# Optimization experiments

Measured on AMD Instinct MI355X. Metric: run time of the kernel, lower is better.

## Reference

```python
import jax, jax.numpy as jnp
import numpy as np

B, S, N, E = 16, 2048, 256, 4096      # batch, tokens, max entities, edges per sample
H, LD, ETR = 512, 16, 768             # hidden_size, label_emb_dim, transformer dim
D = H + LD                            # graph_dim = 528
C1 = 3                                # num_edge_classes + 1
GL = 2                                # gcn_layers
NLBL = 15                             # num_node_classes + 2


def setup_inputs() -> dict:
    key = jax.random.key(0)
    ks = jax.random.split(key, 14)
    s = 0.02
    inp = {}
    inp["emb"] = jax.random.normal(ks[0], (B, S, ETR), jnp.float32)
    inp["ent_indices"] = jax.random.randint(ks[1], (B, S), 0, N + 1)
    inp["ent_labels"] = jax.random.randint(ks[2], (B, N), 0, NLBL)
    inp["edge_index"] = jax.random.randint(ks[3], (B, 2, E), 0, N + 1)
    inp["edge_attr"] = jax.random.randint(ks[4], (B, E), 0, C1)
    inp["cands"] = jax.random.randint(ks[5], (B, N + 1, N + 1), 0, 2).astype(bool)
    inp["W_red"] = jax.random.normal(ks[6], (ETR, H), jnp.float32) * s
    inp["b_red"] = jnp.zeros((H,), jnp.float32)
    inp["emb_label_tbl"] = jax.random.normal(ks[7], (NLBL, LD), jnp.float32) * s
    inp["W_gcn"] = jax.random.normal(ks[8], (C1, GL, D, D), jnp.float32) * s
    inp["b_gcn"] = jnp.zeros((C1, GL, D), jnp.float32)
    inp["W_head"] = jax.random.normal(ks[9], (D, D), jnp.float32) * s
    inp["b_head"] = jnp.zeros((D,), jnp.float32)
    inp["W_tail"] = jax.random.normal(ks[10], (D, D), jnp.float32) * s
    inp["b_tail"] = jnp.zeros((D,), jnp.float32)
    inp["W_out"] = jax.random.normal(ks[11], (D, C1), jnp.float32) * s
    inp["b_out"] = jnp.zeros((C1,), jnp.float32)
    return inp


def _gcn_layer(x, src, dst, w_e, W, b):
    """PyG GCNConv with edge weights w_e (0/1 relation mask) and self loops.
    x: [n, D]; src/dst: [E]; aggregation flow source->target."""
    n = x.shape[0]
    h = x @ W
    deg = jax.ops.segment_sum(w_e, dst, num_segments=n) + 1.0  # +1 self loop
    dinv = jax.lax.rsqrt(deg)
    coef = w_e * dinv[src] * dinv[dst]                         # D^-1/2 A D^-1/2
    agg = jax.ops.segment_sum(coef[:, None] * h[src], dst, num_segments=n)
    return agg + h / deg[:, None] + b                          # self-loop norm = 1/deg


def reference(emb, ent_indices, ent_labels, edge_index, edge_attr, cands,
              W_red, b_red, emb_label_tbl, W_gcn, b_gcn,
              W_head, b_head, W_tail, b_tail, W_out, b_out):
    n_nodes = cands.shape[1]  # max_num_ent + 1
    # fc_reduction of frozen transformer embeddings
    red = emb @ W_red + b_red                                   # [B,S,H]
    # tag-based segment aggregation: max over (mask * emb) == max(segment_max, 0)
    seg_max = jax.vmap(lambda e, ids: jax.ops.segment_max(e, ids, num_segments=n_nodes))(red, ent_indices)
    ent_hidden = jnp.maximum(seg_max, 0.0).at[:, 0, :].set(0.0)  # tag 0 stays zero
    # label embeddings: tag t uses ent_labels[:, t-1]; zeroed where label==0
    lab = emb_label_tbl[ent_labels] * (ent_labels != 0)[..., None].astype(red.dtype)
    lab0 = jnp.broadcast_to(emb_label_tbl[0], (lab.shape[0], 1, lab.shape[-1]))
    label_part = jnp.concatenate([lab0, lab], axis=1)           # [B,n_nodes,LD]
    x0 = jnp.concatenate([label_part, ent_hidden], axis=-1)     # [B,n_nodes,D]
    # multi-relation GCN: per edge class, stacked GCNConv, summed then averaged
    src, dst = edge_index[:, 0], edge_index[:, 1]
    layer_v = jax.vmap(_gcn_layer, in_axes=(0, 0, 0, 0, None, None))
    result = jnp.zeros_like(x0)
    n_cls = W_gcn.shape[0]
    for c in range(n_cls):
        w_e = (edge_attr == c).astype(x0.dtype)
        x = x0
        for l in range(W_gcn.shape[1]):
            x = layer_v(x, src, dst, w_e, W_gcn[c, l], b_gcn[c, l])
        result = result + x
    result = result / n_cls
    # head/tail projections and 'add' pairwise features gated by candidate mask
    x_head = result @ W_head + b_head
    x_tail = result @ W_tail + b_tail
    m = cands[:, :, 1:].astype(x0.dtype)                        # [B,n_nodes,n_nodes-1]
    # fc_out is linear: ((h_i + t_j) * m_ij) @ W + b == m_ij*(hW_i + tW_j) + b
    hW = x_head @ W_out                                         # [B,n_nodes,C1]
    tW = x_tail[:, 1:] @ W_out                                  # [B,n_nodes-1,C1]
    logits = (hW[:, :, None, :] + tW[:, None, :, :]) * m[..., None] + b_out
    return logits  # [B, n_nodes, n_nodes-1, C1] edge-class logits
```

## Files before the change

kernel.cpp:

```cpp
#include <hip/hip_runtime.h>
#include <hip/hip_bf16.h>

typedef unsigned short u16;
typedef __attribute__((ext_vector_type(8))) short short8;
typedef __attribute__((ext_vector_type(4))) float floatx4;

#define B_ 16
#define S_ 2048
#define NNODE 257
#define E_ 4096
#define ETR_ 768
#define H_ 512
#define D_ 528
#define KPAD 544
#define NC 3
#define NROW (B_*NNODE)
#define DD (D_*D_)

#define BM 128
#define BN 128
#define BK 32

__device__ inline u16 f2b(float x) {
    __hip_bfloat16 h = __float2bfloat16(x);
    return *(u16*)&h;
}

__device__ inline void gll16(const u16* g, u16* l) {
    __builtin_amdgcn_global_load_lds(
        (const __attribute__((address_space(1))) void*)g,
        (__attribute__((address_space(3))) void*)l,
        16, 0, 0);
}

__device__ inline int clampi(int v, int hi) { return v < hi ? v : hi; }

__global__ void cvt_bf16(const float* __restrict__ in, u16* __restrict__ out, int n4)
{
    const int i = blockIdx.x * 256 + threadIdx.x;
    if (i < n4) {
        const float4 f = ((const float4*)in)[i];
        ushort4 o;
        o.x = f2b(f.x); o.y = f2b(f.y); o.z = f2b(f.z); o.w = f2b(f.w);
        ((ushort4*)out)[i] = o;
    }
}

__global__ void transpose_cvt(const float* __restrict__ in, u16* __restrict__ out,
                              int R, int Cc, size_t instride, size_t outstride,
                              int opitch)
{
    __shared__ float t[32][33];
    const int z = blockIdx.z;
    const int tx = threadIdx.x & 31, ty = threadIdx.x >> 5;
    const int c0 = blockIdx.x * 32, r0 = blockIdx.y * 32;
    const float* ip = in + z * instride;
    u16* op = out + z * outstride;
#pragma unroll
    for (int i = 0; i < 4; i++) {
        const int r = r0 + ty + i * 8, c = c0 + tx;
        if (r < R && c < Cc) t[ty + i * 8][tx] = ip[(size_t)r * Cc + c];
    }
    __syncthreads();
#pragma unroll
    for (int i = 0; i < 4; i++) {
        const int c = c0 + ty + i * 8, r = r0 + tx;
        if (c < Cc && r < R) op[(size_t)c * opitch + r] = f2b(t[tx][ty + i * 8]);
    }
}

template<int SWZ>
__global__ __launch_bounds__(256)
void gemm_mfma(const u16* __restrict__ A, const u16* __restrict__ Wt,
               float* __restrict__ C, int M, int N, int K, float scale,
               size_t astride, size_t wstride, size_t cstride)
{
    __shared__ u16 SS[8192];
    const int tid = threadIdx.x;
    const int wave = tid >> 6, lane = tid & 63;
    const int quad = lane >> 4, l16 = lane & 15;
    const int z = blockIdx.z;
    int bx = blockIdx.x, by = blockIdx.y;
    if (SWZ) {
        const int lin = blockIdx.x + (blockIdx.y << 2);
        bx = (lin >> 3) & 3;
        by = (lin & 7) + ((lin >> 5) << 3);
    }
    const int m0 = by * BM, n0 = bx * BN;

    floatx4 acc[2][8];
#pragma unroll
    for (int t = 0; t < 2; t++)
#pragma unroll
        for (int u = 0; u < 8; u++)
#pragma unroll
            for (int r = 0; r < 4; r++) acc[t][u][r] = 0.f;

    const int srow = tid >> 2;
    const int scol = (tid & 3) * 8;
    const u16* aP0 = A + z * astride + (size_t)clampi(m0 + srow,      M - 1) * K + scol;
    const u16* aP1 = A + z * astride + (size_t)clampi(m0 + 64 + srow, M - 1) * K + scol;
    const u16* bP0 = Wt + z * wstride + (size_t)clampi(n0 + srow,      N - 1) * K + scol;
    const u16* bP1 = Wt + z * wstride + (size_t)clampi(n0 + 64 + srow, N - 1) * K + scol;
    u16* const ls = &SS[0] + wave * 512;

    for (int k0 = 0; k0 < K; k0 += BK) {
        gll16(aP0 + k0, ls);
        gll16(aP1 + k0, ls + 2048);
        gll16(bP0 + k0, ls + 4096);
        gll16(bP1 + k0, ls + 6144);
        __syncthreads();
        short8 af[2], bfv[8];
        af[0] = *(const short8*)&SS[(wave * 32 + l16) * 32 + quad * 8];
        af[1] = *(const short8*)&SS[(wave * 32 + 16 + l16) * 32 + quad * 8];
#pragma unroll
        for (int u = 0; u < 8; u++)
            bfv[u] = *(const short8*)&SS[4096 + (u * 16 + l16) * 32 + quad * 8];
#pragma unroll
        for (int t = 0; t < 2; t++)
#pragma unroll
            for (int u = 0; u < 8; u++)
                acc[t][u] = __builtin_amdgcn_mfma_f32_16x16x32_bf16(af[t], bfv[u], acc[t][u], 0, 0, 0);
        __syncthreads();
    }

#pragma unroll
    for (int t = 0; t < 2; t++) {
#pragma unroll
        for (int r = 0; r < 4; r++) {
            const int m = m0 + wave * 32 + t * 16 + quad * 4 + r;
            if (m >= M) continue;
#pragma unroll
            for (int u = 0; u < 8; u++) {
                const int n = n0 + u * 16 + l16;
                if (n < N)
                    C[z * cstride + (size_t)m * N + n] = acc[t][u][r] * scale;
            }
        }
    }
}

template<int MODE>
__global__ __launch_bounds__(256)
void gemm64(const float* __restrict__ A, const float* __restrict__ W,
            const float* __restrict__ bias, float* __restrict__ C,
            int M, int N, int K, float scale,
            const int* __restrict__ segidx, float* __restrict__ segout)
{
    __shared__ float Asl[16][68];
    __shared__ float Bsl[16][64];
    const int tid = threadIdx.x;
    const int tx = tid & 15, ty = tid >> 4;
    const int m0 = blockIdx.y * 64, n0 = blockIdx.x * 64;
    const int arow = tid >> 2, acol = (tid & 3) * 4;
    const int brow = tid >> 4, bcol = (tid & 15) * 4;

    float acc[4][4];
#pragma unroll
    for (int i = 0; i < 4; i++)
#pragma unroll
        for (int j = 0; j < 4; j++) acc[i][j] = 0.f;

    for (int kk = 0; kk < K; kk += 16) {
        float4 av = make_float4(0.f, 0.f, 0.f, 0.f);
        if (m0 + arow < M) av = *(const float4*)(A + (size_t)(m0 + arow) * K + kk + acol);
        Asl[acol + 0][arow] = av.x; Asl[acol + 1][arow] = av.y;
        Asl[acol + 2][arow] = av.z; Asl[acol + 3][arow] = av.w;
        float4 bv = make_float4(0.f, 0.f, 0.f, 0.f);
        if (n0 + bcol < N) bv = *(const float4*)(W + (size_t)(kk + brow) * N + n0 + bcol);
        *(float4*)&Bsl[brow][bcol] = bv;
        __syncthreads();
#pragma unroll
        for (int k = 0; k < 16; k++) {
            const float4 a = *(const float4*)&Asl[k][ty * 4];
            const float4 b = *(const float4*)&Bsl[k][tx * 4];
            const float af[4] = { a.x, a.y, a.z, a.w };
            const float bfv[4] = { b.x, b.y, b.z, b.w };
#pragma unroll
            for (int i = 0; i < 4; i++)
#pragma unroll
                for (int j = 0; j < 4; j++) acc[i][j] += af[i] * bfv[j];
        }
        __syncthreads();
    }

#pragma unroll
    for (int i = 0; i < 4; i++) {
        const int m = m0 + ty * 4 + i;
        if (m >= M) continue;
        if (MODE == 1) {
            const int bb = m >> 11;
            const int idx = segidx[m];
            float* const srow = segout + (((size_t)bb * NNODE + idx) << 9);
#pragma unroll
            for (int j = 0; j < 4; j++) {
                const int n = n0 + tx * 4 + j;
                const float v = acc[i][j] + (bias ? bias[n] : 0.f);
                atomicMax(((int*)srow) + n, __float_as_int(v));
            }
        } else {
#pragma unroll
            for (int j = 0; j < 4; j++) {
                const int n = n0 + tx * 4 + j;
                if (n < N) {
                    const float v = acc[i][j] * scale + (bias ? bias[n] : 0.f);
                    C[(size_t)m * N + n] = v;
                }
            }
        }
    }
}

__global__ void rows_csr(const int* __restrict__ ent_indices,
                         int* __restrict__ rptr, int* __restrict__ rlist)
{
    __shared__ int cnt[NNODE];
    const int b = blockIdx.x;
    const int tid = threadIdx.x;
    const int* idx = ent_indices + (size_t)b * S_;
    for (int i = tid; i < NNODE; i += 256) cnt[i] = 0;
    __syncthreads();
    for (int r = tid; r < S_; r += 256) atomicAdd(&cnt[idx[r]], 1);
    __syncthreads();
    if (tid == 0) {
        int run = 0;
        for (int i = 0; i < NNODE; i++) { const int c = cnt[i]; cnt[i] = run; run += c; }
    }
    __syncthreads();
    for (int i = tid; i < NNODE; i += 256) rptr[b * (NNODE + 1) + i] = cnt[i];
    if (tid == 0) rptr[b * (NNODE + 1) + NNODE] = S_;
    __syncthreads();
    for (int r = tid; r < S_; r += 256) {
        const int pos = atomicAdd(&cnt[idx[r]], 1);
        rlist[(size_t)b * S_ + pos] = r;
    }
}

__global__ __launch_bounds__(256)
void segmax_kernel(const float* __restrict__ redC, const int* __restrict__ rptr,
                   const int* __restrict__ rlist, const float* __restrict__ b_red,
                   float* __restrict__ seg)
{
    const int bn = blockIdx.x;
    const int b = bn / NNODE, n = bn % NNODE;
    const int tid = threadIdx.x;
    const int start = rptr[b * (NNODE + 1) + n];
    const int end   = rptr[b * (NNODE + 1) + n + 1];
    float m0 = -INFINITY, m1 = -INFINITY;
    const int* rl = rlist + (size_t)b * S_;
    for (int i = start; i < end; i++) {
        const float* row = redC + ((size_t)b * S_ + rl[i]) * H_;
        m0 = fmaxf(m0, row[tid]);
        m1 = fmaxf(m1, row[tid + 256]);
    }
    float* out = seg + (size_t)bn * H_;
    out[tid]       = fmaxf(m0 + b_red[tid], 0.f);
    out[tid + 256] = fmaxf(m1 + b_red[tid + 256], 0.f);
}

template<int OUTB>
__global__ void build_x0(const float* __restrict__ seg, const int* __restrict__ ent_labels,
                         const float* __restrict__ tbl, float* __restrict__ x0f,
                         u16* __restrict__ x0b)
{
    const int bn = blockIdx.x;
    const int b = bn / NNODE, n = bn % NNODE;
    const int CMAX = OUTB ? KPAD : D_;
    for (int col = threadIdx.x; col < CMAX; col += blockDim.x) {
        float v;
        if (col >= D_) {
            v = 0.f;
        } else if (col < 16) {
            if (n == 0) v = tbl[col];
            else {
                const int lab = ent_labels[b * (NNODE - 1) + (n - 1)];
                v = (lab != 0) ? tbl[lab * 16 + col] : 0.f;
            }
        } else {
            v = (n == 0) ? 0.f : seg[(((size_t)b * NNODE + n) << 9) + (col - 16)];
        }
        if (OUTB) x0b[(size_t)bn * KPAD + col] = f2b(v);
        else      x0f[(size_t)bn * D_ + col] = v;
    }
}

__global__ void csr_build(const int* __restrict__ edge_index, const int* __restrict__ edge_attr,
                          float* __restrict__ degf, int* __restrict__ csr_ptr,
                          int2* __restrict__ csr_sc)
{
    __shared__ int cnt[NC * NNODE];
    __shared__ float dinvl[NC * NNODE];
    const int b = blockIdx.x;
    const int tid = threadIdx.x;
    const int* src = edge_index + (size_t)b * 2 * E_;
    const int* dst = src + E_;
    const int* attr = edge_attr + (size_t)b * E_;

    for (int i = tid; i < NC * NNODE; i += 256) cnt[i] = 0;
    __syncthreads();
    for (int e = tid; e < E_; e += 256) atomicAdd(&cnt[attr[e] * NNODE + dst[e]], 1);
    __syncthreads();
    for (int i = tid; i < NC * NNODE; i += 256) {
        const float d = (float)cnt[i] + 1.0f;
        degf[(size_t)b * NC * NNODE + i] = d;
        dinvl[i] = rsqrtf(d);
    }
    __syncthreads();
    if (tid == 0) {
        int run = 0;
        for (int i = 0; i < NC * NNODE; i++) { const int c = cnt[i]; cnt[i] = run; run += c; }
    }
    __syncthreads();
    for (int i = tid; i < NC * NNODE; i += 256) csr_ptr[(size_t)b * NC * NNODE + i] = cnt[i];
    __syncthreads();
    for (int e = tid; e < E_; e += 256) {
        const int a = attr[e], d = dst[e], s = src[e];
        const int pos = atomicAdd(&cnt[a * NNODE + d], 1);
        const float cf = dinvl[a * NNODE + s] * dinvl[a * NNODE + d];
        csr_sc[(size_t)b * E_ + pos] = make_int2(s, __float_as_int(cf));
    }
}

template<int OUT>
__global__ __launch_bounds__(256)
void gcn_gather(const float* __restrict__ h, size_t hstride,
                const float* __restrict__ degf,
                const int* __restrict__ csr_ptr, const int2* __restrict__ csr_sc,
                const float* __restrict__ bias_base, size_t bias_stride,
                float* __restrict__ outf, u16* __restrict__ outb, size_t ostride,
                int cls0)
{
    const int bn = blockIdx.x;
    const int cls = cls0 + blockIdx.y;
    const int b = bn / NNODE, n = bn % NNODE;
    const int tid = threadIdx.x;
    const int base = b * NC * NNODE + cls * NNODE + n;
    const float d = degf[base];
    const int start = csr_ptr[base];
    const int cnt = (int)d - 1;
    const float inv = 1.0f / d;
    const float* hp = h + blockIdx.y * hstride;
    const float* bias = bias_base + cls * bias_stride;
    const float* hrow = hp + (size_t)bn * D_;
    const int c0 = tid, c1 = tid + 256, c2 = tid + 512;
    float a0 = hrow[c0] * inv + bias[c0];
    float a1 = hrow[c1] * inv + bias[c1];
    float a2 = (c2 < D_) ? hrow[c2] * inv + bias[c2] : 0.f;
    const int2* scp = csr_sc + (size_t)b * E_ + start;
    for (int i = 0; i < cnt; i++) {
        const int2 sc = scp[i];
        const float cf = __int_as_float(sc.y);
        const float* hs = hp + ((size_t)b * NNODE + sc.x) * D_;
        a0 += cf * hs[c0];
        a1 += cf * hs[c1];
        if (c2 < D_) a2 += cf * hs[c2];
    }
    if (OUT == 0) {
        u16* orow = outb + blockIdx.y * ostride + (size_t)bn * KPAD;
        orow[c0] = f2b(a0); orow[c1] = f2b(a1); if (c2 < D_) orow[c2] = f2b(a2);
        if (tid >= 16 && tid < 32) orow[512 + tid] = 0;
    } else if (OUT == 1) {
        float* orow = outf + (size_t)bn * D_;
        orow[c0] += a0; orow[c1] += a1; if (c2 < D_) orow[c2] += a2;
    } else if (OUT == 2) {
        float* orow = outf + (size_t)bn * D_;
        orow[c0] = a0; orow[c1] = a1; if (c2 < D_) orow[c2] = a2;
    } else {
        float* orow = outf + (size_t)bn * D_;
        atomicAdd(&orow[c0], a0); atomicAdd(&orow[c1], a1);
        if (c2 < D_) atomicAdd(&orow[c2], a2);
    }
}

__global__ void rowdot3(const float* __restrict__ x, const float* __restrict__ w,
                        float* __restrict__ out)
{
    const int row = blockIdx.x;
    const int lane = threadIdx.x;
    float a0 = 0.f, a1 = 0.f, a2 = 0.f;
    for (int d = lane; d < D_; d += 64) {
        const float xv = x[(size_t)row * D_ + d];
        a0 += xv * w[d * 3 + 0];
        a1 += xv * w[d * 3 + 1];
        a2 += xv * w[d * 3 + 2];
    }
#pragma unroll
    for (int off = 32; off > 0; off >>= 1) {
        a0 += __shfl_down(a0, off, 64);
        a1 += __shfl_down(a1, off, 64);
        a2 += __shfl_down(a2, off, 64);
    }
    if (lane == 0) {
        out[(size_t)row * 3 + 0] = a0;
        out[(size_t)row * 3 + 1] = a1;
        out[(size_t)row * 3 + 2] = a2;
    }
}

__global__ void rowdot6(const float* __restrict__ x, const float* __restrict__ Whw,
                        const float* __restrict__ Wtw, const float* __restrict__ bias6,
                        float* __restrict__ hw, float* __restrict__ tw)
{
    const int row = blockIdx.x;
    const int lane = threadIdx.x;
    float h0 = 0.f, h1 = 0.f, h2 = 0.f, t0 = 0.f, t1 = 0.f, t2 = 0.f;
    for (int d = lane; d < D_; d += 64) {
        const float xv = x[(size_t)row * D_ + d] * (1.f / 3.f);
        h0 += xv * Whw[d * 3 + 0]; h1 += xv * Whw[d * 3 + 1]; h2 += xv * Whw[d * 3 + 2];
        t0 += xv * Wtw[d * 3 + 0]; t1 += xv * Wtw[d * 3 + 1]; t2 += xv * Wtw[d * 3 + 2];
    }
#pragma unroll
    for (int off = 32; off > 0; off >>= 1) {
        h0 += __shfl_down(h0, off, 64); h1 += __shfl_down(h1, off, 64); h2 += __shfl_down(h2, off, 64);
        t0 += __shfl_down(t0, off, 64); t1 += __shfl_down(t1, off, 64); t2 += __shfl_down(t2, off, 64);
    }
    if (lane == 0) {
        hw[(size_t)row * 3 + 0] = h0 + bias6[0];
        hw[(size_t)row * 3 + 1] = h1 + bias6[1];
        hw[(size_t)row * 3 + 2] = h2 + bias6[2];
        tw[(size_t)row * 3 + 0] = t0 + bias6[3];
        tw[(size_t)row * 3 + 1] = t1 + bias6[4];
        tw[(size_t)row * 3 + 2] = t2 + bias6[5];
    }
}

__global__ __launch_bounds__(256)
void final_logits(const float* __restrict__ hw, const float* __restrict__ tw,
                  const int* __restrict__ cands, const float* __restrict__ b_out,
                  float* __restrict__ out)
{
    const int bi = blockIdx.x;
    const int b = bi / NNODE;
    const int j = threadIdx.x;
    const float h0 = hw[bi * 3 + 0], h1 = hw[bi * 3 + 1], h2 = hw[bi * 3 + 2];
    const int tj = b * NNODE + 1 + j;
    const float t0 = tw[tj * 3 + 0], t1 = tw[tj * 3 + 1], t2 = tw[tj * 3 + 2];
    const float m = (cands[(size_t)bi * NNODE + 1 + j] != 0) ? 1.f : 0.f;
    const float bo0 = b_out[0], bo1 = b_out[1], bo2 = b_out[2];
    const size_t o = ((size_t)bi * 256 + j) * 3;
    out[o + 0] = (h0 + t0) * m + bo0;
    out[o + 1] = (h1 + t1) * m + bo1;
    out[o + 2] = (h2 + t2) * m + bo2;
}

extern "C" void kernel_launch(void* const* d_in, const int* in_sizes, int n_in,
                              void* d_out, int out_size, void* d_ws, size_t ws_size,
                              hipStream_t stream)
{
    const float* emb       = (const float*)d_in[0];
    const int* ent_indices = (const int*)d_in[1];
    const int* ent_labels  = (const int*)d_in[2];
    const int* edge_index  = (const int*)d_in[3];
    const int* edge_attr   = (const int*)d_in[4];
    const int* cands       = (const int*)d_in[5];
    const float* W_red     = (const float*)d_in[6];
    const float* b_red     = (const float*)d_in[7];
    const float* tbl       = (const float*)d_in[8];
    const float* W_gcn     = (const float*)d_in[9];
    const float* b_gcn     = (const float*)d_in[10];
    const float* W_head    = (const float*)d_in[11];
    const float* b_head    = (const float*)d_in[12];
    const float* W_tail    = (const float*)d_in[13];
    const float* b_tail    = (const float*)d_in[14];
    const float* W_out     = (const float*)d_in[15];
    const float* b_out     = (const float*)d_in[16];

    char* ws = (char*)d_ws;
    size_t off = 0;
    auto alloc = [&](size_t nbytes) -> char* {
        char* p = ws + off; off = (off + nbytes + 255) & ~(size_t)255; return p;
    };
    const size_t ROWB  = (size_t)NROW * D_ * sizeof(float);
    const size_t RD    = (size_t)NROW * D_;
    const size_t RD2   = (size_t)NROW * KPAD;
    const size_t WGZ   = (size_t)2 * D_ * KPAD;

    char* R0      = alloc((size_t)B_ * S_ * ETR_ * sizeof(u16));
    u16*  emb_bf  = (u16*)R0;
    float* hbuf   = (float*)R0;
    u16*  x1b     = (u16*)(R0 + 3 * ROWB);
    float* seg    = (float*)alloc((size_t)B_ * NNODE * H_ * 4);
    float* redC   = (float*)alloc((size_t)B_ * S_ * H_ * 4);
    int*  rptr    = (int*)alloc((size_t)B_ * (NNODE + 1) * 4);
    int*  rlist   = (int*)alloc((size_t)B_ * S_ * 4);
    u16*  x0b     = (u16*)alloc((size_t)NROW * KPAD * sizeof(u16));
    float* result = (float*)alloc(ROWB);
    u16*  wredT   = (u16*)alloc((size_t)H_ * ETR_ * sizeof(u16));
    u16*  wgcnT   = (u16*)alloc((size_t)NC * WGZ * sizeof(u16));
    float* Whw    = (float*)alloc((size_t)D_ * 3 * 4);
    float* Wtw    = (float*)alloc((size_t)D_ * 3 * 4);
    float* bias6  = (float*)alloc(6 * 4);
    float* degf   = (float*)alloc((size_t)B_ * NC * NNODE * 4);
    float* hwp    = (float*)alloc((size_t)NROW * 3 * 4);
    float* twp    = (float*)alloc((size_t)NROW * 3 * 4);
    int* csr_ptr  = (int*)alloc((size_t)B_ * NC * NNODE * 4);
    int2* csr_sc  = (int2*)alloc((size_t)B_ * E_ * 8);
    const bool fast = (ws_size >= off);

    if (fast) {
        const int n4e = (B_ * S_ * ETR_) / 4;
        cvt_bf16<<<(n4e + 255) / 256, 256, 0, stream>>>(emb, emb_bf, n4e);
        transpose_cvt<<<dim3(16, 24, 1), 256, 0, stream>>>(W_red, wredT, ETR_, H_, 0, 0, ETR_);
        hipMemsetAsync(wgcnT, 0, (size_t)NC * WGZ * sizeof(u16), stream);
        transpose_cvt<<<dim3(17, 17, 6), 256, 0, stream>>>(W_gcn, wgcnT, D_, D_, DD, (size_t)D_ * KPAD, KPAD);
        hipMemsetAsync(result, 0, ROWB, stream);

        rowdot3<<<D_, 64, 0, stream>>>(W_head, W_out, Whw);
        rowdot3<<<D_, 64, 0, stream>>>(W_tail, W_out, Wtw);
        rowdot3<<<1, 64, 0, stream>>>(b_head, W_out, bias6);
        rowdot3<<<1, 64, 0, stream>>>(b_tail, W_out, bias6 + 3);

        rows_csr<<<B_, 256, 0, stream>>>(ent_indices, rptr, rlist);

        gemm_mfma<1><<<dim3(H_ / BN, (B_ * S_) / BM, 1), 256, 0, stream>>>(
            emb_bf, wredT, redC, B_ * S_, H_, ETR_, 1.f, 0, 0, 0);
        segmax_kernel<<<B_ * NNODE, 256, 0, stream>>>(redC, rptr, rlist, b_red, seg);

        build_x0<1><<<NROW, 256, 0, stream>>>(seg, ent_labels, tbl, nullptr, x0b);
        csr_build<<<B_, 256, 0, stream>>>(edge_index, edge_attr, degf, csr_ptr, csr_sc);

        dim3 gmm((D_ + BN - 1) / BN, (NROW + BM - 1) / BM, NC);
        gemm_mfma<0><<<gmm, 256, 0, stream>>>(
            x0b, wgcnT, hbuf, NROW, D_, KPAD, 1.f, 0, WGZ, RD);
        gcn_gather<0><<<dim3(NROW, NC), 256, 0, stream>>>(
            hbuf, RD, degf, csr_ptr, csr_sc, b_gcn, (size_t)2 * D_,
            nullptr, x1b, RD2, 0);
        gemm_mfma<0><<<gmm, 256, 0, stream>>>(
            x1b, wgcnT + (size_t)D_ * KPAD, hbuf, NROW, D_, KPAD, 1.f, RD2, WGZ, RD);
        gcn_gather<3><<<dim3(NROW, NC), 256, 0, stream>>>(
            hbuf, RD, degf, csr_ptr, csr_sc, b_gcn + D_, (size_t)2 * D_,
            result, nullptr, 0, 0);

        rowdot6<<<NROW, 64, 0, stream>>>(result, Whw, Wtw, bias6, hwp, twp);
        final_logits<<<NROW, 256, 0, stream>>>(hwp, twp, cands, b_out, (float*)d_out);
        return;
    }

    off = 0;
    float* bufA = (float*)alloc(ROWB);
    float* bufB = (float*)alloc(ROWB);
    float* bufC = (float*)alloc(ROWB);
    float* bufD = (float*)alloc(ROWB);
    degf = (float*)alloc((size_t)B_ * NC * NNODE * 4);
    hwp  = (float*)alloc((size_t)NROW * 3 * 4);
    twp  = (float*)alloc((size_t)NROW * 3 * 4);
    csr_ptr = (int*)alloc((size_t)B_ * NC * NNODE * 4);
    csr_sc  = (int2*)alloc((size_t)B_ * E_ * 8);

    hipMemsetAsync(bufA, 0, (size_t)B_ * NNODE * H_ * 4, stream);
    hipMemsetAsync(bufD, 0, ROWB, stream);
    gemm64<1><<<dim3(H_ / 64, (B_ * S_) / 64), 256, 0, stream>>>(
        emb, W_red, b_red, nullptr, B_ * S_, H_, ETR_, 1.f, ent_indices, bufA);
    build_x0<0><<<NROW, 256, 0, stream>>>(bufA, ent_labels, tbl, bufB, nullptr);
    csr_build<<<B_, 256, 0, stream>>>(edge_index, edge_attr, degf, csr_ptr, csr_sc);
    dim3 gridG((D_ + 63) / 64, (NROW + 63) / 64);
    for (int c = 0; c < NC; c++) {
        gemm64<0><<<gridG, 256, 0, stream>>>(bufB, W_gcn + (size_t)(c * 2 + 0) * DD,
            nullptr, bufA, NROW, D_, D_, 1.f, nullptr, nullptr);
        gcn_gather<2><<<dim3(NROW, 1), 256, 0, stream>>>(bufA, 0, degf, csr_ptr, csr_sc,
            b_gcn, (size_t)2 * D_, bufC, nullptr, 0, c);
        gemm64<0><<<gridG, 256, 0, stream>>>(bufC, W_gcn + (size_t)(c * 2 + 1) * DD,
            nullptr, bufA, NROW, D_, D_, 1.f, nullptr, nullptr);
        gcn_gather<1><<<dim3(NROW, 1), 256, 0, stream>>>(bufA, 0, degf, csr_ptr, csr_sc,
            b_gcn + D_, (size_t)2 * D_, bufD, nullptr, 0, c);
    }
    gemm64<0><<<gridG, 256, 0, stream>>>(bufD, W_head, b_head, bufB,
        NROW, D_, D_, 1.f / 3.f, nullptr, nullptr);
    gemm64<0><<<gridG, 256, 0, stream>>>(bufD, W_tail, b_tail, bufC,
        NROW, D_, D_, 1.f / 3.f, nullptr, nullptr);
    rowdot3<<<NROW, 64, 0, stream>>>(bufB, W_out, hwp);
    rowdot3<<<NROW, 64, 0, stream>>>(bufC, W_out, twp);
    final_logits<<<NROW, 256, 0, stream>>>(hwp, twp, cands, b_out, (float*)d_out);
}
```

Before: 442.4 us.

## Emit bf16 reduction GEMM output, fuse segmax with x0 build, drop atomics

The reduction GEMM now writes bf16 instead of fp32, which halves the 64MB intermediate that segmax reads. Segment max is fused with the label-embedding and x0 construction into one kernel that writes bf16 x0 directly. The final GCN gather writes per-class outputs to separate buffers instead of using atomics, and rowdot6 sums the three classes itself, so the result memset is no longer needed. The four rowdot3 setup launches are merged into one, and the edge list is software-prefetched in the gather loop. Rounding the reduction output to bf16 adds precision loss before the max.

New measurement: 413.7 us. -6.5%, faster.

```diff
diff --git a/kernel.cpp b/kernel.cpp
--- a/kernel.cpp
+++ b/kernel.cpp
@@ -69,10 +69,10 @@
     }
 }
 
-template<int SWZ>
+template<int SWZ, int OB16>
 __global__ __launch_bounds__(256)
 void gemm_mfma(const u16* __restrict__ A, const u16* __restrict__ Wt,
-               float* __restrict__ C, int M, int N, int K, float scale,
+               void* __restrict__ Cv, int M, int N, int K, float scale,
                size_t astride, size_t wstride, size_t cstride)
 {
     __shared__ u16 SS[8192];
@@ -133,8 +133,15 @@
 #pragma unroll
             for (int u = 0; u < 8; u++) {
                 const int n = n0 + u * 16 + l16;
-                if (n < N)
-                    C[z * cstride + (size_t)m * N + n] = acc[t][u][r] * scale;
+                if (n < N) {
+                    if (OB16) {
+                        u16* Cb = (u16*)Cv;
+                        Cb[z * cstride + (size_t)m * N + n] = f2b(acc[t][u][r] * scale);
+                    } else {
+                        float* Cf = (float*)Cv;
+                        Cf[z * cstride + (size_t)m * N + n] = acc[t][u][r] * scale;
+                    }
+                }
             }
         }
     }
@@ -237,25 +244,44 @@
 }
 
 __global__ __launch_bounds__(256)
-void segmax_kernel(const float* __restrict__ redC, const int* __restrict__ rptr,
-                   const int* __restrict__ rlist, const float* __restrict__ b_red,
-                   float* __restrict__ seg)
+void segmax_x0(const u16* __restrict__ redC, const int* __restrict__ rptr,
+               const int* __restrict__ rlist, const float* __restrict__ b_red,
+               const int* __restrict__ ent_labels, const float* __restrict__ tbl,
+               u16* __restrict__ x0b)
 {
     const int bn = blockIdx.x;
     const int b = bn / NNODE, n = bn % NNODE;
     const int tid = threadIdx.x;
+    const int c0 = tid * 2;
     const int start = rptr[b * (NNODE + 1) + n];
-    const int end   = rptr[b * (NNODE + 1) + n + 1];
+    const int end   = (n == 0) ? start : rptr[b * (NNODE + 1) + n + 1];
     float m0 = -INFINITY, m1 = -INFINITY;
     const int* rl = rlist + (size_t)b * S_;
     for (int i = start; i < end; i++) {
-        const float* row = redC + ((size_t)b * S_ + rl[i]) * H_;
-        m0 = fmaxf(m0, row[tid]);
-        m1 = fmaxf(m1, row[tid + 256]);
-    }
-    float* out = seg + (size_t)bn * H_;
-    out[tid]       = fmaxf(m0 + b_red[tid], 0.f);
-    out[tid + 256] = fmaxf(m1 + b_red[tid + 256], 0.f);
+        const u16* row = redC + ((size_t)b * S_ + rl[i]) * H_;
+        const unsigned v = *(const unsigned*)(row + c0);
+        m0 = fmaxf(m0, __uint_as_float((v & 0xffffu) << 16));
+        m1 = fmaxf(m1, __uint_as_float(v & 0xffff0000u));
+    }
+    float h0, h1;
+    if (n == 0) { h0 = 0.f; h1 = 0.f; }
+    else {
+        h0 = fmaxf(m0 + b_red[c0], 0.f);
+        h1 = fmaxf(m1 + b_red[c0 + 1], 0.f);
+    }
+    u16* orow = x0b + (size_t)bn * KPAD;
+    *(unsigned*)(orow + 16 + c0) = (unsigned)f2b(h0) | ((unsigned)f2b(h1) << 16);
+    if (tid < 16) {
+        float v;
+        if (n == 0) v = tbl[tid];
+        else {
+            const int lab = ent_labels[b * (NNODE - 1) + (n - 1)];
+            v = (lab != 0) ? tbl[lab * 16 + tid] : 0.f;
+        }
+        orow[tid] = f2b(v);
+    } else if (tid < 32) {
+        orow[512 + tid] = 0;
+    }
 }
 
 template<int OUTB>
@@ -347,10 +373,12 @@
     float a1 = hrow[c1] * inv + bias[c1];
     float a2 = (c2 < D_) ? hrow[c2] * inv + bias[c2] : 0.f;
     const int2* scp = csr_sc + (size_t)b * E_ + start;
+    int2 sc = (cnt > 0) ? scp[0] : make_int2(0, 0);
     for (int i = 0; i < cnt; i++) {
-        const int2 sc = scp[i];
-        const float cf = __int_as_float(sc.y);
-        const float* hs = hp + ((size_t)b * NNODE + sc.x) * D_;
+        const int2 cur = sc;
+        if (i + 1 < cnt) sc = scp[i + 1];
+        const float cf = __int_as_float(cur.y);
+        const float* hs = hp + ((size_t)b * NNODE + cur.x) * D_;
         a0 += cf * hs[c0];
         a1 += cf * hs[c1];
         if (c2 < D_) a2 += cf * hs[c2];
@@ -363,7 +391,7 @@
         float* orow = outf + (size_t)bn * D_;
         orow[c0] += a0; orow[c1] += a1; if (c2 < D_) orow[c2] += a2;
     } else if (OUT == 2) {
-        float* orow = outf + (size_t)bn * D_;
+        float* orow = outf + blockIdx.y * ostride + (size_t)bn * D_;
         orow[c0] = a0; orow[c1] = a1; if (c2 < D_) orow[c2] = a2;
     } else {
         float* orow = outf + (size_t)bn * D_;
@@ -397,15 +425,49 @@
     }
 }
 
-__global__ void rowdot6(const float* __restrict__ x, const float* __restrict__ Whw,
-                        const float* __restrict__ Wtw, const float* __restrict__ bias6,
-                        float* __restrict__ hw, float* __restrict__ tw)
-{
-    const int row = blockIdx.x;
+__global__ void prep_heads(const float* __restrict__ W_head, const float* __restrict__ W_tail,
+                           const float* __restrict__ b_head, const float* __restrict__ b_tail,
+                           const float* __restrict__ W_out,
+                           float* __restrict__ Whw, float* __restrict__ Wtw,
+                           float* __restrict__ bias6)
+{
+    const int r = blockIdx.x;
     const int lane = threadIdx.x;
+    const float* x; float* o;
+    if (r < D_)            { x = W_head + (size_t)r * D_;        o = Whw + (size_t)r * 3; }
+    else if (r < 2 * D_)   { x = W_tail + (size_t)(r - D_) * D_; o = Wtw + (size_t)(r - D_) * 3; }
+    else if (r == 2 * D_)  { x = b_head;                         o = bias6; }
+    else                   { x = b_tail;                         o = bias6 + 3; }
+    float a0 = 0.f, a1 = 0.f, a2 = 0.f;
+    for (int d = lane; d < D_; d += 64) {
+        const float xv = x[d];
+        a0 += xv * W_out[d * 3 + 0];
+        a1 += xv * W_out[d * 3 + 1];
+        a2 += xv * W_out[d * 3 + 2];
+    }
+#pragma unroll
+    for (int off = 32; off > 0; off >>= 1) {
+        a0 += __shfl_down(a0, off, 64);
+        a1 += __shfl_down(a1, off, 64);
+        a2 += __shfl_down(a2, off, 64);
+    }
+    if (lane == 0) { o[0] = a0; o[1] = a1; o[2] = a2; }
+}
+
+__global__ __launch_bounds__(256)
+void rowdot6(const float* __restrict__ x3, size_t zstride,
+             const float* __restrict__ Whw, const float* __restrict__ Wtw,
+             const float* __restrict__ bias6,
+             float* __restrict__ hw, float* __restrict__ tw)
+{
+    const int row = blockIdx.x * 4 + (threadIdx.x >> 6);
+    const int lane = threadIdx.x & 63;
+    const float* p0 = x3 + (size_t)row * D_;
+    const float* p1 = p0 + zstride;
+    const float* p2 = p1 + zstride;
     float h0 = 0.f, h1 = 0.f, h2 = 0.f, t0 = 0.f, t1 = 0.f, t2 = 0.f;
     for (int d = lane; d < D_; d += 64) {
-        const float xv = x[(size_t)row * D_ + d] * (1.f / 3.f);
+        const float xv = (p0[d] + p1[d] + p2[d]) * (1.f / 3.f);
         h0 += xv * Whw[d * 3 + 0]; h1 += xv * Whw[d * 3 + 1]; h2 += xv * Whw[d * 3 + 2];
         t0 += xv * Wtw[d * 3 + 0]; t1 += xv * Wtw[d * 3 + 1]; t2 += xv * Wtw[d * 3 + 2];
     }
@@ -479,12 +541,12 @@
     u16*  emb_bf  = (u16*)R0;
     float* hbuf   = (float*)R0;
     u16*  x1b     = (u16*)(R0 + 3 * ROWB);
-    float* seg    = (float*)alloc((size_t)B_ * NNODE * H_ * 4);
-    float* redC   = (float*)alloc((size_t)B_ * S_ * H_ * 4);
+    char* R1      = alloc((size_t)B_ * S_ * H_ * sizeof(u16));
+    u16*  redC    = (u16*)R1;
+    float* result3 = (float*)R1;
     int*  rptr    = (int*)alloc((size_t)B_ * (NNODE + 1) * 4);
     int*  rlist   = (int*)alloc((size_t)B_ * S_ * 4);
     u16*  x0b     = (u16*)alloc((size_t)NROW * KPAD * sizeof(u16));
-    float* result = (float*)alloc(ROWB);
     u16*  wredT   = (u16*)alloc((size_t)H_ * ETR_ * sizeof(u16));
     u16*  wgcnT   = (u16*)alloc((size_t)NC * WGZ * sizeof(u16));
     float* Whw    = (float*)alloc((size_t)D_ * 3 * 4);
@@ -503,35 +565,32 @@
         transpose_cvt<<<dim3(16, 24, 1), 256, 0, stream>>>(W_red, wredT, ETR_, H_, 0, 0, ETR_);
         hipMemsetAsync(wgcnT, 0, (size_t)NC * WGZ * sizeof(u16), stream);
         transpose_cvt<<<dim3(17, 17, 6), 256, 0, stream>>>(W_gcn, wgcnT, D_, D_, DD, (size_t)D_ * KPAD, KPAD);
-        hipMemsetAsync(result, 0, ROWB, stream);
-
-        rowdot3<<<D_, 64, 0, stream>>>(W_head, W_out, Whw);
-        rowdot3<<<D_, 64, 0, stream>>>(W_tail, W_out, Wtw);
-        rowdot3<<<1, 64, 0, stream>>>(b_head, W_out, bias6);
-        rowdot3<<<1, 64, 0, stream>>>(b_tail, W_out, bias6 + 3);
+
+        prep_heads<<<2 * D_ + 2, 64, 0, stream>>>(W_head, W_tail, b_head, b_tail, W_out,
+                                                  Whw, Wtw, bias6);
 
         rows_csr<<<B_, 256, 0, stream>>>(ent_indices, rptr, rlist);
 
-        gemm_mfma<1><<<dim3(H_ / BN, (B_ * S_) / BM, 1), 256, 0, stream>>>(
+        gemm_mfma<1, 1><<<dim3(H_ / BN, (B_ * S_) / BM, 1), 256, 0, stream>>>(
             emb_bf, wredT, redC, B_ * S_, H_, ETR_, 1.f, 0, 0, 0);
-        segmax_kernel<<<B_ * NNODE, 256, 0, stream>>>(redC, rptr, rlist, b_red, seg);
-
-        build_x0<1><<<NROW, 256, 0, stream>>>(seg, ent_labels, tbl, nullptr, x0b);
+        segmax_x0<<<B_ * NNODE, 256, 0, stream>>>(redC, rptr, rlist, b_red,
+                                                  ent_labels, tbl, x0b);
+
         csr_build<<<B_, 256, 0, stream>>>(edge_index, edge_attr, degf, csr_ptr, csr_sc);
 
         dim3 gmm((D_ + BN - 1) / BN, (NROW + BM - 1) / BM, NC);
-        gemm_mfma<0><<<gmm, 256, 0, stream>>>(
+        gemm_mfma<0, 0><<<gmm, 256, 0, stream>>>(
             x0b, wgcnT, hbuf, NROW, D_, KPAD, 1.f, 0, WGZ, RD);
         gcn_gather<0><<<dim3(NROW, NC), 256, 0, stream>>>(
             hbuf, RD, degf, csr_ptr, csr_sc, b_gcn, (size_t)2 * D_,
             nullptr, x1b, RD2, 0);
-        gemm_mfma<0><<<gmm, 256, 0, stream>>>(
+        gemm_mfma<0, 0><<<gmm, 256, 0, stream>>>(
             x1b, wgcnT + (size_t)D_ * KPAD, hbuf, NROW, D_, KPAD, 1.f, RD2, WGZ, RD);
-        gcn_gather<3><<<dim3(NROW, NC), 256, 0, stream>>>(
+        gcn_gather<2><<<dim3(NROW, NC), 256, 0, stream>>>(
             hbuf, RD, degf, csr_ptr, csr_sc, b_gcn + D_, (size_t)2 * D_,
-            result, nullptr, 0, 0);
-
-        rowdot6<<<NROW, 64, 0, stream>>>(result, Whw, Wtw, bias6, hwp, twp);
+            result3, nullptr, RD, 0);
+
+        rowdot6<<<NROW / 4, 256, 0, stream>>>(result3, RD, Whw, Wtw, bias6, hwp, twp);
         final_logits<<<NROW, 256, 0, stream>>>(hwp, twp, cands, b_out, (float*)d_out);
         return;
     }
```
